# Optimization experiments

Measured on AMD Instinct MI355X. Metric: run time of the kernel, lower is better.

The kernel has to match this reference:

```python
import jax, jax.numpy as jnp
import numpy as np

N_NODES = 100000
N_EDGES = 400000
D = 128           # vector_dim
N_GRAPHS = 4096
N_LAYERS = 5
IN_FEAT = 11


def setup_inputs() -> dict:
    key = jax.random.key(0)
    ks = jax.random.split(key, 6)
    x = jax.random.uniform(ks[0], (N_NODES, IN_FEAT), dtype=jnp.float32)
    edge_index = jax.random.randint(ks[1], (2, N_EDGES), 0, N_NODES, dtype=jnp.int64)
    batch = jnp.sort(jax.random.randint(ks[2], (N_NODES,), 0, N_GRAPHS, dtype=jnp.int64))
    # expansion Linear(11, D)
    We = jax.random.normal(ks[3], (IN_FEAT, D), dtype=jnp.float32) * (1.0 / np.sqrt(IN_FEAT))
    be = jnp.zeros((D,), dtype=jnp.float32)
    # stacked GCNConv weights/biases for 5 layers
    Wg = jax.random.normal(ks[4], (N_LAYERS, D, D), dtype=jnp.float32) * (1.0 / np.sqrt(D))
    bg = jnp.zeros((N_LAYERS, D), dtype=jnp.float32)
    return {"x": x, "edge_index": edge_index, "batch": batch, "num_graphs": N_GRAPHS,
            "We": We, "be": be, "Wg": Wg, "bg": bg}


def reference(x, edge_index, batch, num_graphs, We, be, Wg, bg):
    n = x.shape[0]
    src, dst = edge_index[0], edge_index[1]
    # GCNConv(improved=True): self-loop weight 2 -> deg[i] = in_degree + 2
    deg = jax.ops.segment_sum(jnp.ones((src.shape[0],), x.dtype), dst, num_segments=n) + 2.0
    dinv = deg ** -0.5
    enorm = dinv[src] * dinv[dst]          # per-edge symmetric norm [E]
    self_norm = 2.0 * dinv * dinv          # self-loop contribution [N]

    h = jnp.log(x + 1.0) @ We + be         # expansion [N, D]
    for l in range(Wg.shape[0]):
        t = h @ Wg[l]                      # [N, D]
        agg = jax.ops.segment_sum(t[src] * enorm[:, None], dst, num_segments=n)
        agg = agg + self_norm[:, None] * t + bg[l]
        h = h + jax.nn.relu(agg)           # residual; dropout = identity (eval)
    return jax.ops.segment_sum(h, batch, num_segments=num_graphs)  # global_add_pool [G, D]
```

## Files before the change

kernel.cpp:

```cpp
#include <hip/hip_runtime.h>
#include <hip/hip_bf16.h>

#define NN 100000
#define NE 400000
#define DD 128
#define NG 4096
#define NL 5
#define NF 11
#define GROWS 100096

typedef __attribute__((ext_vector_type(8))) __bf16 bf16x8;
typedef __attribute__((ext_vector_type(4))) float f32x4;


__global__ void deg_kernel(const int* __restrict__ ei, int* __restrict__ deg) {
    int e = blockIdx.x * 256 + threadIdx.x;
    if (e < NE) atomicAdd(&deg[ei[NE + e]], 1);
}

__global__ void scan1_kernel(const int* __restrict__ deg, int* __restrict__ off,
                             int* __restrict__ bsums) {
    __shared__ int lds[256];
    int tid = threadIdx.x, b = blockIdx.x;
    int base = b * 1024 + tid * 4;
    int v[4];
#pragma unroll
    for (int q = 0; q < 4; ++q) {
        int i = base + q;
        v[q] = (i < NN) ? deg[i] : 0;
    }
    int s = v[0] + v[1] + v[2] + v[3];
    lds[tid] = s;
    __syncthreads();
    for (int o = 1; o < 256; o <<= 1) {
        int t2 = (tid >= o) ? lds[tid - o] : 0;
        __syncthreads();
        lds[tid] += t2;
        __syncthreads();
    }
    int p = lds[tid] - s;
#pragma unroll
    for (int q = 0; q < 4; ++q) {
        int i = base + q;
        if (i < NN) off[i] = p;
        p += v[q];
    }
    if (tid == 255) bsums[b] = lds[255];
}

__global__ void scan2_kernel(int* __restrict__ bsums, int nb) {
    __shared__ int lds[128];
    int tid = threadIdx.x;
    int v = (tid < nb) ? bsums[tid] : 0;
    lds[tid] = v;
    __syncthreads();
    for (int o = 1; o < 128; o <<= 1) {
        int t2 = (tid >= o) ? lds[tid - o] : 0;
        __syncthreads();
        lds[tid] += t2;
        __syncthreads();
    }
    if (tid < nb) bsums[tid] = lds[tid] - v;
}

__global__ void finish_kernel(int* __restrict__ off, const int* __restrict__ bsums,
                              const int* __restrict__ deg, float* __restrict__ dinv) {
    int i = blockIdx.x * 256 + threadIdx.x;
    if (i == 0) off[NN] = NE;
    if (i < NN) {
        off[i] += bsums[i >> 10];
        dinv[i] = rsqrtf((float)deg[i] + 2.0f);
    }
}

__global__ void fill_kernel(const int* __restrict__ ei, const int* __restrict__ off,
                            int* __restrict__ cursor, int2* __restrict__ csr,
                            const float* __restrict__ dinv) {
    int e = blockIdx.x * 256 + threadIdx.x;
    if (e >= NE) return;
    int s = ei[e];
    int d = ei[NE + e];
    int pos = off[d] + atomicAdd(&cursor[d], 1);
    csr[pos] = make_int2(s, __float_as_int(dinv[s] * dinv[d]));
}


__global__ void wpack_kernel(const float* __restrict__ Wg, unsigned short* __restrict__ whi,
                             unsigned short* __restrict__ wlo) {
    int t = blockIdx.x * 256 + threadIdx.x;
    int l = t >> 14, r = t & 16383;
    int k = r >> 7, n = r & 127;
    float w = Wg[(size_t)l * 16384 + k * 128 + n];
    __bf16 hb = (__bf16)w;
    float lo = w - (float)hb;
    __bf16 lb = (__bf16)lo;
    int ft = n >> 4, kc = k >> 5, lane = (((k >> 3) & 3) << 4) | (n & 15), i = k & 7;
    size_t idx = (size_t)l * 16384 + (((ft * 4 + kc) * 64 + lane) * 8 + i);
    whi[idx] = __builtin_bit_cast(unsigned short, hb);
    wlo[idx] = __builtin_bit_cast(unsigned short, lb);
}


__global__ void logx_kernel(const float* __restrict__ x, float* __restrict__ lx) {
    int t = blockIdx.x * 256 + threadIdx.x;
    if (t < NN * NF) lx[t] = __logf(x[t] + 1.0f);
}

__global__ __launch_bounds__(256) void expand_kernel(const float* __restrict__ lx,
                                                     const float* __restrict__ We,
                                                     const float* __restrict__ be,
                                                     float* __restrict__ h) {
    __shared__ float ls[2 * NF];
    const int tid = threadIdx.x;
    const int node0 = blockIdx.x * 2;
    if (tid < 2 * NF) ls[tid] = lx[(size_t)node0 * NF + tid];
    __syncthreads();
    const int row = tid >> 7, j = tid & 127;
    float acc = be[j];
#pragma unroll
    for (int f = 0; f < NF; ++f) {
        acc = fmaf(ls[row * NF + f], We[f * DD + j], acc);
    }
    h[(size_t)(node0 + row) * DD + j] = acc;
}


__global__ __launch_bounds__(256) void agg_kernel(const float* __restrict__ h,
                                                  float* __restrict__ g,
                                                  const int* __restrict__ off,
                                                  const int2* __restrict__ csr,
                                                  const float* __restrict__ dinv) {
    const int tid = threadIdx.x;
    const int node = blockIdx.x * 8 + (tid >> 5);
    const int jj = tid & 31;
    const float4* __restrict__ h4 = (const float4*)h;

    float di = dinv[node];
    float sn = 2.0f * di * di;
    float4 hv = h4[(size_t)node * 32 + jj];
    float4 acc = make_float4(sn * hv.x, sn * hv.y, sn * hv.z, sn * hv.w);

    const int e0 = off[node];
    const int e1 = off[node + 1];
#pragma unroll 1
    for (int e = e0; e < e1; e += 8) {
        const int eL = e1 - 1;
        int2 r[8];
#pragma unroll
        for (int q = 0; q < 8; ++q) r[q] = csr[min(e + q, eL)];
        float4 v[8];
#pragma unroll
        for (int q = 0; q < 8; ++q) v[q] = h4[(size_t)r[q].x * 32 + jj];
#pragma unroll
        for (int q = 0; q < 8; ++q) {
            float w = (e + q < e1) ? __int_as_float(r[q].y) : 0.f;
            acc.x = fmaf(w, v[q].x, acc.x);
            acc.y = fmaf(w, v[q].y, acc.y);
            acc.z = fmaf(w, v[q].z, acc.z);
            acc.w = fmaf(w, v[q].w, acc.w);
        }
    }
    ((float4*)g)[(size_t)node * 32 + jj] = acc;
}


__global__ __launch_bounds__(256) void mfma_gemm(const float* __restrict__ g,
                                                 float* __restrict__ h,
                                                 const unsigned short* __restrict__ whi,
                                                 const unsigned short* __restrict__ wlo,
                                                 const float* __restrict__ b) {
    const int lane = threadIdx.x & 63;
    const int wv = threadIdx.x >> 6;
    const int node = blockIdx.x * 64 + wv * 16 + (lane & 15);
    const int kg = lane >> 4;

    float4 gf[8];
    {
        const float* gp = g + (size_t)node * DD + kg * 8;
#pragma unroll
        for (int kc = 0; kc < 4; ++kc) {
            gf[kc * 2]     = *(const float4*)(gp + kc * 32);
            gf[kc * 2 + 1] = *(const float4*)(gp + kc * 32 + 4);
        }
    }

    bf16x8 gh[4], gl[4];
#pragma unroll
    for (int kc = 0; kc < 4; ++kc) {
        float t[8] = {gf[kc * 2].x,     gf[kc * 2].y,     gf[kc * 2].z,     gf[kc * 2].w,
                      gf[kc * 2 + 1].x, gf[kc * 2 + 1].y, gf[kc * 2 + 1].z, gf[kc * 2 + 1].w};
#pragma unroll
        for (int i = 0; i < 8; ++i) {
            __bf16 hi = (__bf16)t[i];
            float lo = t[i] - (float)hi;
            gh[kc][i] = hi;
            gl[kc][i] = (__bf16)lo;
        }
    }

    f32x4 c[8];
#pragma unroll
    for (int ft = 0; ft < 8; ++ft) c[ft] = (f32x4){0.f, 0.f, 0.f, 0.f};

#pragma unroll
    for (int kc = 0; kc < 4; ++kc) {
#pragma unroll
        for (int ft = 0; ft < 8; ++ft) {
            size_t boff = (size_t)(((ft * 4 + kc) * 64 + lane) * 8);
            bf16x8 wh = *(const bf16x8*)(whi + boff);
            bf16x8 wl = *(const bf16x8*)(wlo + boff);
            c[ft] = __builtin_amdgcn_mfma_f32_16x16x32_bf16(wh, gh[kc], c[ft], 0, 0, 0);
            c[ft] = __builtin_amdgcn_mfma_f32_16x16x32_bf16(wl, gh[kc], c[ft], 0, 0, 0);
            c[ft] = __builtin_amdgcn_mfma_f32_16x16x32_bf16(wh, gl[kc], c[ft], 0, 0, 0);
        }
    }

    if (node < NN) {
        const int f0 = kg * 4;
#pragma unroll
        for (int ft = 0; ft < 8; ++ft) {
            size_t o = (size_t)node * DD + ft * 16 + f0;
            float4 hv = *(const float4*)(h + o);
            float4 bv = *(const float4*)(b + ft * 16 + f0);
            hv.x += fmaxf(c[ft][0] + bv.x, 0.f);
            hv.y += fmaxf(c[ft][1] + bv.y, 0.f);
            hv.z += fmaxf(c[ft][2] + bv.z, 0.f);
            hv.w += fmaxf(c[ft][3] + bv.w, 0.f);
            *(float4*)(h + o) = hv;
        }
    }
}


__global__ void pool_kernel(const float* __restrict__ h, const int* __restrict__ batch,
                            float* __restrict__ out) {
    int j = threadIdx.x;
    int n0 = blockIdx.x * 64;
    float acc = 0.f;
    int prev = -1;
    for (int n = 0; n < 64; ++n) {
        int i = n0 + n;
        if (i >= NN) break;
        int bi = batch[i];
        if (bi != prev) {
            if (prev >= 0) atomicAdd(&out[(size_t)prev * DD + j], acc);
            acc = 0.f;
            prev = bi;
        }
        acc += h[(size_t)i * DD + j];
    }
    if (prev >= 0) atomicAdd(&out[(size_t)prev * DD + j], acc);
}


static inline size_t align_up(size_t x, size_t a) { return (x + a - 1) & ~(a - 1); }

extern "C" void kernel_launch(void* const* d_in, const int* in_sizes, int n_in,
                              void* d_out, int out_size, void* d_ws, size_t ws_size,
                              hipStream_t stream) {
    const float* x   = (const float*)d_in[0];
    const int*   ei  = (const int*)d_in[1];
    const int*   bat = (const int*)d_in[2];
    const float* We  = (const float*)d_in[4];
    const float* be  = (const float*)d_in[5];
    const float* Wg  = (const float*)d_in[6];
    const float* bg  = (const float*)d_in[7];
    float* out = (float*)d_out;

    char* p = (char*)d_ws;
    size_t o = 0;
    float* h = (float*)(p + o);       o = align_up(o + (size_t)NN * DD * 4, 512);
    float* g = (float*)(p + o);       o = align_up(o + (size_t)GROWS * DD * 4, 512);
    float* dinv = (float*)(p + o);    o = align_up(o + (size_t)NN * 4, 512);
    int* deg = (int*)(p + o);         o = align_up(o + (size_t)NN * 4, 512);
    int* cursor = (int*)(p + o);      o = align_up(o + (size_t)NN * 4, 512);
    int* off = (int*)(p + o);         o = align_up(o + (size_t)(NN + 1) * 4, 512);
    int* bsums = (int*)(p + o);       o = align_up(o + 512, 512);
    int2* csr = (int2*)(p + o);       o = align_up(o + (size_t)NE * 8, 512);
    unsigned short* whi = (unsigned short*)(p + o); o = align_up(o + (size_t)NL * 16384 * 2, 512);
    unsigned short* wlo = (unsigned short*)(p + o); o = align_up(o + (size_t)NL * 16384 * 2, 512);
    float* lx = (float*)(p + o);      o = align_up(o + (size_t)NN * NF * 4, 512);
    (void)ws_size; (void)in_sizes; (void)n_in; (void)out_size;

    const int GRID_E = (NE + 255) / 256;
    const int GRID_SCAN1 = (NN + 1023) / 1024;
    const int GRID_N256 = (NN + 255) / 256;
    const int GRID_LOGX = (NN * NF + 255) / 256;
    const int GRID_EXP = NN / 2;
    const int GRID_AGG = NN / 8;
    const int GRID_GEMM = GROWS / 64;
    const int GRID_POOL = (NN + 63) / 64;
    const int GRID_WPACK = NL * 16384 / 256;

    hipMemsetAsync(deg, 0, (size_t)NN * 4, stream);
    hipMemsetAsync(cursor, 0, (size_t)NN * 4, stream);
    hipMemsetAsync(out, 0, (size_t)NG * DD * 4, stream);

    deg_kernel<<<GRID_E, 256, 0, stream>>>(ei, deg);
    scan1_kernel<<<GRID_SCAN1, 256, 0, stream>>>(deg, off, bsums);
    scan2_kernel<<<1, 128, 0, stream>>>(bsums, GRID_SCAN1);
    finish_kernel<<<GRID_N256, 256, 0, stream>>>(off, bsums, deg, dinv);
    fill_kernel<<<GRID_E, 256, 0, stream>>>(ei, off, cursor, csr, dinv);
    wpack_kernel<<<GRID_WPACK, 256, 0, stream>>>(Wg, whi, wlo);

    logx_kernel<<<GRID_LOGX, 256, 0, stream>>>(x, lx);
    expand_kernel<<<GRID_EXP, 256, 0, stream>>>(lx, We, be, h);

    for (int l = 0; l < NL; ++l) {
        agg_kernel<<<GRID_AGG, 256, 0, stream>>>(h, g, off, csr, dinv);
        mfma_gemm<<<GRID_GEMM, 256, 0, stream>>>(g, h,
                                                 whi + (size_t)l * 16384,
                                                 wlo + (size_t)l * 16384,
                                                 bg + (size_t)l * DD);
    }

    pool_kernel<<<GRID_POOL, 128, 0, stream>>>(h, bat, out);
}
```

Measured before the change: 584.1 us.

## Fuse log into expand, shrink agg unroll, and tile GEMM over two node tiles

The separate log(x+1) kernel is folded into the expansion kernel, which removes one launch and an intermediate buffer round trip. The aggregation loop now processes 4 edges per iteration instead of 8, cutting register pressure and wasted clamped loads at the cost of fewer loads in flight. The MFMA GEMM now computes two 16-node tiles per wave, so each loaded weight fragment is reused twice and the grid is halved, at the cost of more accumulator registers.

```diff
diff --git a/kernel.cpp b/kernel.cpp
--- a/kernel.cpp
+++ b/kernel.cpp
@@ -101,19 +101,14 @@
 }
 
 
-__global__ void logx_kernel(const float* __restrict__ x, float* __restrict__ lx) {
-    int t = blockIdx.x * 256 + threadIdx.x;
-    if (t < NN * NF) lx[t] = __logf(x[t] + 1.0f);
-}
-
-__global__ __launch_bounds__(256) void expand_kernel(const float* __restrict__ lx,
+__global__ __launch_bounds__(256) void expand_kernel(const float* __restrict__ x,
                                                      const float* __restrict__ We,
                                                      const float* __restrict__ be,
                                                      float* __restrict__ h) {
     __shared__ float ls[2 * NF];
     const int tid = threadIdx.x;
     const int node0 = blockIdx.x * 2;
-    if (tid < 2 * NF) ls[tid] = lx[(size_t)node0 * NF + tid];
+    if (tid < 2 * NF) ls[tid] = __logf(x[(size_t)node0 * NF + tid] + 1.0f);
     __syncthreads();
     const int row = tid >> 7, j = tid & 127;
     float acc = be[j];
@@ -143,22 +138,28 @@
     const int e0 = off[node];
     const int e1 = off[node + 1];
 #pragma unroll 1
-    for (int e = e0; e < e1; e += 8) {
+    for (int e = e0; e < e1; e += 4) {
         const int eL = e1 - 1;
-        int2 r[8];
-#pragma unroll
-        for (int q = 0; q < 8; ++q) r[q] = csr[min(e + q, eL)];
-        float4 v[8];
-#pragma unroll
-        for (int q = 0; q < 8; ++q) v[q] = h4[(size_t)r[q].x * 32 + jj];
-#pragma unroll
-        for (int q = 0; q < 8; ++q) {
-            float w = (e + q < e1) ? __int_as_float(r[q].y) : 0.f;
-            acc.x = fmaf(w, v[q].x, acc.x);
-            acc.y = fmaf(w, v[q].y, acc.y);
-            acc.z = fmaf(w, v[q].z, acc.z);
-            acc.w = fmaf(w, v[q].w, acc.w);
-        }
+        int2 r0 = csr[e];
+        int2 r1 = csr[min(e + 1, eL)];
+        int2 r2 = csr[min(e + 2, eL)];
+        int2 r3 = csr[min(e + 3, eL)];
+        float4 v0 = h4[(size_t)r0.x * 32 + jj];
+        float4 v1 = h4[(size_t)r1.x * 32 + jj];
+        float4 v2 = h4[(size_t)r2.x * 32 + jj];
+        float4 v3 = h4[(size_t)r3.x * 32 + jj];
+        float w0 = __int_as_float(r0.y);
+        float w1 = (e + 1 < e1) ? __int_as_float(r1.y) : 0.f;
+        float w2 = (e + 2 < e1) ? __int_as_float(r2.y) : 0.f;
+        float w3 = (e + 3 < e1) ? __int_as_float(r3.y) : 0.f;
+        acc.x = fmaf(w0, v0.x, acc.x); acc.y = fmaf(w0, v0.y, acc.y);
+        acc.z = fmaf(w0, v0.z, acc.z); acc.w = fmaf(w0, v0.w, acc.w);
+        acc.x = fmaf(w1, v1.x, acc.x); acc.y = fmaf(w1, v1.y, acc.y);
+        acc.z = fmaf(w1, v1.z, acc.z); acc.w = fmaf(w1, v1.w, acc.w);
+        acc.x = fmaf(w2, v2.x, acc.x); acc.y = fmaf(w2, v2.y, acc.y);
+        acc.z = fmaf(w2, v2.z, acc.z); acc.w = fmaf(w2, v2.w, acc.w);
+        acc.x = fmaf(w3, v3.x, acc.x); acc.y = fmaf(w3, v3.y, acc.y);
+        acc.z = fmaf(w3, v3.z, acc.z); acc.w = fmaf(w3, v3.w, acc.w);
     }
     ((float4*)g)[(size_t)node * 32 + jj] = acc;
 }
@@ -171,36 +172,33 @@
                                                  const float* __restrict__ b) {
     const int lane = threadIdx.x & 63;
     const int wv = threadIdx.x >> 6;
-    const int node = blockIdx.x * 64 + wv * 16 + (lane & 15);
+    const int nbase = blockIdx.x * 128 + wv * 32 + (lane & 15);
     const int kg = lane >> 4;
 
-    float4 gf[8];
-    {
-        const float* gp = g + (size_t)node * DD + kg * 8;
+    bf16x8 gh[2][4], gl[2][4];
+#pragma unroll
+    for (int nt = 0; nt < 2; ++nt) {
+        const float* gp = g + (size_t)(nbase + nt * 16) * DD + kg * 8;
 #pragma unroll
         for (int kc = 0; kc < 4; ++kc) {
-            gf[kc * 2]     = *(const float4*)(gp + kc * 32);
-            gf[kc * 2 + 1] = *(const float4*)(gp + kc * 32 + 4);
+            float4 f0 = *(const float4*)(gp + kc * 32);
+            float4 f1 = *(const float4*)(gp + kc * 32 + 4);
+            float t[8] = {f0.x, f0.y, f0.z, f0.w, f1.x, f1.y, f1.z, f1.w};
+#pragma unroll
+            for (int i = 0; i < 8; ++i) {
+                __bf16 hi = (__bf16)t[i];
+                float lo = t[i] - (float)hi;
+                gh[nt][kc][i] = hi;
+                gl[nt][kc][i] = (__bf16)lo;
+            }
         }
     }
 
-    bf16x8 gh[4], gl[4];
-#pragma unroll
-    for (int kc = 0; kc < 4; ++kc) {
-        float t[8] = {gf[kc * 2].x,     gf[kc * 2].y,     gf[kc * 2].z,     gf[kc * 2].w,
-                      gf[kc * 2 + 1].x, gf[kc * 2 + 1].y, gf[kc * 2 + 1].z, gf[kc * 2 + 1].w};
-#pragma unroll
-        for (int i = 0; i < 8; ++i) {
-            __bf16 hi = (__bf16)t[i];
-            float lo = t[i] - (float)hi;
-            gh[kc][i] = hi;
-            gl[kc][i] = (__bf16)lo;
-        }
-    }
-
-    f32x4 c[8];
-#pragma unroll
-    for (int ft = 0; ft < 8; ++ft) c[ft] = (f32x4){0.f, 0.f, 0.f, 0.f};
+    f32x4 c[2][8];
+#pragma unroll
+    for (int nt = 0; nt < 2; ++nt)
+#pragma unroll
+        for (int ft = 0; ft < 8; ++ft) c[nt][ft] = (f32x4){0.f, 0.f, 0.f, 0.f};
 
 #pragma unroll
     for (int kc = 0; kc < 4; ++kc) {
@@ -209,24 +207,31 @@
             size_t boff = (size_t)(((ft * 4 + kc) * 64 + lane) * 8);
             bf16x8 wh = *(const bf16x8*)(whi + boff);
             bf16x8 wl = *(const bf16x8*)(wlo + boff);
-            c[ft] = __builtin_amdgcn_mfma_f32_16x16x32_bf16(wh, gh[kc], c[ft], 0, 0, 0);
-            c[ft] = __builtin_amdgcn_mfma_f32_16x16x32_bf16(wl, gh[kc], c[ft], 0, 0, 0);
-            c[ft] = __builtin_amdgcn_mfma_f32_16x16x32_bf16(wh, gl[kc], c[ft], 0, 0, 0);
+#pragma unroll
+            for (int nt = 0; nt < 2; ++nt) {
+                c[nt][ft] = __builtin_amdgcn_mfma_f32_16x16x32_bf16(wh, gh[nt][kc], c[nt][ft], 0, 0, 0);
+                c[nt][ft] = __builtin_amdgcn_mfma_f32_16x16x32_bf16(wl, gh[nt][kc], c[nt][ft], 0, 0, 0);
+                c[nt][ft] = __builtin_amdgcn_mfma_f32_16x16x32_bf16(wh, gl[nt][kc], c[nt][ft], 0, 0, 0);
+            }
         }
     }
 
-    if (node < NN) {
-        const int f0 = kg * 4;
-#pragma unroll
-        for (int ft = 0; ft < 8; ++ft) {
-            size_t o = (size_t)node * DD + ft * 16 + f0;
-            float4 hv = *(const float4*)(h + o);
-            float4 bv = *(const float4*)(b + ft * 16 + f0);
-            hv.x += fmaxf(c[ft][0] + bv.x, 0.f);
-            hv.y += fmaxf(c[ft][1] + bv.y, 0.f);
-            hv.z += fmaxf(c[ft][2] + bv.z, 0.f);
-            hv.w += fmaxf(c[ft][3] + bv.w, 0.f);
-            *(float4*)(h + o) = hv;
+    const int f0 = kg * 4;
+#pragma unroll
+    for (int nt = 0; nt < 2; ++nt) {
+        const int node = nbase + nt * 16;
+        if (node < NN) {
+#pragma unroll
+            for (int ft = 0; ft < 8; ++ft) {
+                size_t o = (size_t)node * DD + ft * 16 + f0;
+                float4 hv = *(const float4*)(h + o);
+                float4 bv = *(const float4*)(b + ft * 16 + f0);
+                hv.x += fmaxf(c[nt][ft][0] + bv.x, 0.f);
+                hv.y += fmaxf(c[nt][ft][1] + bv.y, 0.f);
+                hv.z += fmaxf(c[nt][ft][2] + bv.z, 0.f);
+                hv.w += fmaxf(c[nt][ft][3] + bv.w, 0.f);
+                *(float4*)(h + o) = hv;
+            }
         }
     }
 }
@@ -279,16 +284,14 @@
     int2* csr = (int2*)(p + o);       o = align_up(o + (size_t)NE * 8, 512);
     unsigned short* whi = (unsigned short*)(p + o); o = align_up(o + (size_t)NL * 16384 * 2, 512);
     unsigned short* wlo = (unsigned short*)(p + o); o = align_up(o + (size_t)NL * 16384 * 2, 512);
-    float* lx = (float*)(p + o);      o = align_up(o + (size_t)NN * NF * 4, 512);
     (void)ws_size; (void)in_sizes; (void)n_in; (void)out_size;
 
     const int GRID_E = (NE + 255) / 256;
     const int GRID_SCAN1 = (NN + 1023) / 1024;
     const int GRID_N256 = (NN + 255) / 256;
-    const int GRID_LOGX = (NN * NF + 255) / 256;
     const int GRID_EXP = NN / 2;
     const int GRID_AGG = NN / 8;
-    const int GRID_GEMM = GROWS / 64;
+    const int GRID_GEMM = GROWS / 128;
     const int GRID_POOL = (NN + 63) / 64;
     const int GRID_WPACK = NL * 16384 / 256;
 
@@ -303,8 +306,7 @@
     fill_kernel<<<GRID_E, 256, 0, stream>>>(ei, off, cursor, csr, dinv);
     wpack_kernel<<<GRID_WPACK, 256, 0, stream>>>(Wg, whi, wlo);
 
-    logx_kernel<<<GRID_LOGX, 256, 0, stream>>>(x, lx);
-    expand_kernel<<<GRID_EXP, 256, 0, stream>>>(lx, We, be, h);
+    expand_kernel<<<GRID_EXP, 256, 0, stream>>>(x, We, be, h);
 
     for (int l = 0; l < NL; ++l) {
         agg_kernel<<<GRID_AGG, 256, 0, stream>>>(h, g, off, csr, dinv);
```

After: 603.0 us. +3.2%, slower.
